# Kernel optimization log

Hardware: AMD Instinct MI355X
Metric: run time of the kernel (lower is better)

The kernel has to match this reference:

```python
import jax, jax.numpy as jnp
import numpy as np

B, S, D_IN, D_MODEL, H = 4, 2048, 1024, 1024, 16
D_HEAD = D_MODEL // H


def setup_inputs() -> dict:
    key = jax.random.key(0)
    ks = jax.random.split(key, 10)
    sc_in = 1.0 / np.sqrt(D_IN)
    sc_md = 1.0 / np.sqrt(D_MODEL)
    return {
        "X1": jax.random.normal(ks[0], (B, S, D_IN), jnp.float32),
        "X2": jax.random.normal(ks[1], (B, S, D_IN), jnp.float32),
        "Wq": jax.random.uniform(ks[2], (D_IN, D_MODEL), jnp.float32, -sc_in, sc_in),
        "bq": jax.random.uniform(ks[3], (D_MODEL,), jnp.float32, -sc_in, sc_in),
        "Wk": jax.random.uniform(ks[4], (D_IN, D_MODEL), jnp.float32, -sc_in, sc_in),
        "bk": jax.random.uniform(ks[5], (D_MODEL,), jnp.float32, -sc_in, sc_in),
        "Wv": jax.random.uniform(ks[6], (D_IN, D_MODEL), jnp.float32, -sc_in, sc_in),
        "bv": jax.random.uniform(ks[7], (D_MODEL,), jnp.float32, -sc_in, sc_in),
        "Wo": jax.random.uniform(ks[8], (D_MODEL, D_MODEL), jnp.float32, -sc_md, sc_md),
        "bo": jax.random.uniform(ks[9], (D_MODEL,), jnp.float32, -sc_md, sc_md),
    }


def _split_heads(x):
    b, s, _ = x.shape
    return x.reshape(b, s, H, D_HEAD).transpose(0, 2, 1, 3)  # [B,H,S,Dh]


def reference(X1, X2, Wq, bq, Wk, bk, Wv, bv, Wo, bo):
    Q = _split_heads(X1 @ Wq + bq)
    K = _split_heads(X2 @ Wk + bk)
    V = _split_heads(X2 @ Wv + bv)
    scale = 1.0 / np.sqrt(D_HEAD).astype(np.float32)
    # unfused attention: full [B,H,S,S] score matrix, as in the source
    scores = jnp.einsum("bhqd,bhkd->bhqk", Q, K) * scale
    attn = jax.nn.softmax(scores, axis=-1)
    out = jnp.einsum("bhqk,bhkd->bhqd", attn, V)
    out = out.transpose(0, 2, 1, 3).reshape(X1.shape[0], X1.shape[1], D_MODEL)
    return out @ Wo + bo
```

## Files before the change

### kernel.cpp

```cpp
#include <hip/hip_runtime.h>
#include <math.h>

typedef __bf16 bf16x8 __attribute__((ext_vector_type(8)));
typedef float  f32x4  __attribute__((ext_vector_type(4)));
typedef unsigned int uint2v __attribute__((ext_vector_type(2)));
typedef unsigned short u16;
typedef unsigned int   u32;

__device__ __forceinline__ u16 f2bf(float f) {
    u32 u = __builtin_bit_cast(u32, f);
    u32 r = (u + 0x7FFFu + ((u >> 16) & 1u)) >> 16;
    return (u16)r;
}

__device__ __forceinline__ u32 cvtpk_bf16(float lo, float hi) {
    u32 r;
    asm("v_cvt_pk_bf16_f32 %0, %1, %2" : "=v"(r) : "v"(lo), "v"(hi));
    return r;
}

#if __has_builtin(__builtin_amdgcn_exp2f)
__device__ __forceinline__ float fast_exp2(float x) { return __builtin_amdgcn_exp2f(x); }
#else
__device__ __forceinline__ float fast_exp2(float x) { return exp2f(x); }
#endif

__device__ __forceinline__ void mfma_16x16x16(f32x4& acc, uint2v a, uint2v b) {
    asm("v_mfma_f32_16x16x16_bf16 %0, %1, %2, %0" : "+v"(acc) : "v"(a), "v"(b));
}

__device__ __forceinline__ void gll16(const void* g, void* l) {
    __builtin_amdgcn_global_load_lds(
        (const __attribute__((address_space(1))) u32*)g,
        (__attribute__((address_space(3))) u32*)l, 16, 0, 0);
}

__device__ __forceinline__ f32x4 zero4() {
    f32x4 z; z[0] = 0.f; z[1] = 0.f; z[2] = 0.f; z[3] = 0.f; return z;
}

__global__ void cvt2_kernel(const float* __restrict__ in0, const float* __restrict__ in1,
                            u16* __restrict__ o0, u16* __restrict__ o1, int n) {
    const float* in = blockIdx.y ? in1 : in0;
    u16* out = blockIdx.y ? o1 : o0;
    int stride = gridDim.x * blockDim.x * 4;
    for (int i = (blockIdx.x * blockDim.x + threadIdx.x) * 4; i < n; i += stride) {
        float4 v = *(const float4*)&in[i];
        ushort4 r;
        r.x = f2bf(v.x); r.y = f2bf(v.y); r.z = f2bf(v.z); r.w = f2bf(v.w);
        *(ushort4*)&out[i] = r;
    }
}

__global__ void transpose_w(const float* __restrict__ W0, const float* __restrict__ W1,
                            const float* __restrict__ W2, const float* __restrict__ W3,
                            u16* __restrict__ T0, u16* __restrict__ T1,
                            u16* __restrict__ T2, u16* __restrict__ T3) {
    const float* W = blockIdx.z == 0 ? W0 : blockIdx.z == 1 ? W1 : blockIdx.z == 2 ? W2 : W3;
    u16*         T = blockIdx.z == 0 ? T0 : blockIdx.z == 1 ? T1 : blockIdx.z == 2 ? T2 : T3;
    __shared__ float tile[32][33];
    const int tx = threadIdx.x, ty = threadIdx.y;
    const int n0 = blockIdx.x * 32, k0 = blockIdx.y * 32;
#pragma unroll
    for (int i = 0; i < 4; ++i)
        tile[ty + 8 * i][tx] = W[(size_t)(k0 + ty + 8 * i) * 1024 + n0 + tx];
    __syncthreads();
#pragma unroll
    for (int i = 0; i < 4; ++i)
        T[(size_t)(n0 + ty + 8 * i) * 1024 + k0 + tx] = f2bf(tile[tx][ty + 8 * i]);
}

__global__ __launch_bounds__(256, 2)
void gemm_qkv(const u16* __restrict__ A1, const u16* __restrict__ A2,
              const u16* __restrict__ BTq, const u16* __restrict__ BTk, const u16* __restrict__ BTv,
              const float* __restrict__ bq, const float* __restrict__ bk, const float* __restrict__ bv,
              u16* __restrict__ qb, u16* __restrict__ kb, u16* __restrict__ vtb) {
    __shared__ u16 Alds[128 * 64];
    __shared__ u16 Blds[128 * 64];

    const int z = blockIdx.z;
    const u16* A    = z == 0 ? A1 : A2;
    const u16* BT   = z == 0 ? BTq : z == 1 ? BTk : BTv;
    const float* bias = z == 0 ? bq : z == 1 ? bk : bv;

    const int t = threadIdx.x;
    const int lane = t & 63, wid = t >> 6;
    const int wr = wid >> 1, wc = wid & 1;

    int wg = blockIdx.y * gridDim.x + blockIdx.x;
    const int cpx = 512 >> 3;
    wg = (wg & 7) * cpx + (wg >> 3);
    const int bx = wg & 7, by = wg >> 3;

    const int m0 = by * 128, n0 = bx * 128;

    f32x4 acc[4][4];
#pragma unroll
    for (int i = 0; i < 4; ++i)
#pragma unroll
        for (int j = 0; j < 4; ++j) acc[i][j] = zero4();

    const int srow = t >> 3;
    const int scol = (t & 7) * 8;
    const int lr = lane & 15;
    const int lk = (lane >> 4) * 8;

    for (int ko = 0; ko < 1024; ko += 64) {
#pragma unroll
        for (int i = 0; i < 4; ++i) {
            gll16(A  + (size_t)(m0 + srow + 32 * i) * 1024 + ko + scol, &Alds[(srow + 32 * i) * 64 + scol]);
            gll16(BT + (size_t)(n0 + srow + 32 * i) * 1024 + ko + scol, &Blds[(srow + 32 * i) * 64 + scol]);
        }
        __syncthreads();
#pragma unroll
        for (int kk = 0; kk < 2; ++kk) {
            bf16x8 a[4], b[4];
#pragma unroll
            for (int mi = 0; mi < 4; ++mi)
                a[mi] = *(const bf16x8*)&Alds[(wr * 64 + mi * 16 + lr) * 64 + kk * 32 + lk];
#pragma unroll
            for (int ni = 0; ni < 4; ++ni)
                b[ni] = *(const bf16x8*)&Blds[(wc * 64 + ni * 16 + lr) * 64 + kk * 32 + lk];
#pragma unroll
            for (int mi = 0; mi < 4; ++mi)
#pragma unroll
                for (int ni = 0; ni < 4; ++ni)
                    acc[mi][ni] = __builtin_amdgcn_mfma_f32_16x16x32_bf16(a[mi], b[ni], acc[mi][ni], 0, 0, 0);
        }
        __syncthreads();
    }

    const float KSC = (z == 1) ? 0.125f * 1.44269504f : 1.0f;

#pragma unroll
    for (int mi = 0; mi < 4; ++mi) {
#pragma unroll
        for (int ni = 0; ni < 4; ++ni) {
#pragma unroll
            for (int r = 0; r < 4; ++r) {
                const int m = m0 + wr * 64 + mi * 16 + (lane >> 4) * 4 + r;
                const int n = n0 + wc * 64 + ni * 16 + lr;
                const float v = (acc[mi][ni][r] + bias[n]) * KSC;
                const int b = m >> 11, s = m & 2047;
                const int hh = n >> 6, d = n & 63;
                const int bh = (b << 4) | hh;
                if (z <= 1) {
                    u16* dst = z == 0 ? qb : kb;
                    dst[((size_t)bh * 2048 + s) * 64 + d] = f2bf(v);
                } else {
                    vtb[((size_t)bh * 64 + d) * 2048 + s] = f2bf(v);
                }
            }
        }
    }
}

__global__ __launch_bounds__(256, 2)
void gemm_out(const u16* __restrict__ A, const u16* __restrict__ BT,
              const float* __restrict__ bias, float* __restrict__ out) {
    __shared__ u16 Alds[128 * 64];
    __shared__ u16 Blds[128 * 64];

    const int t = threadIdx.x;
    const int lane = t & 63, wid = t >> 6;
    const int wr = wid >> 1, wc = wid & 1;

    int wg = blockIdx.y * gridDim.x + blockIdx.x;
    const int cpx = 512 >> 3;
    wg = (wg & 7) * cpx + (wg >> 3);
    const int bx = wg & 7, by = wg >> 3;

    const int m0 = by * 128, n0 = bx * 128;

    f32x4 acc[4][4];
#pragma unroll
    for (int i = 0; i < 4; ++i)
#pragma unroll
        for (int j = 0; j < 4; ++j) acc[i][j] = zero4();

    const int srow = t >> 3;
    const int scol = (t & 7) * 8;
    const int lr = lane & 15;
    const int lk = (lane >> 4) * 8;

    for (int ko = 0; ko < 1024; ko += 64) {
#pragma unroll
        for (int i = 0; i < 4; ++i) {
            gll16(A  + (size_t)(m0 + srow + 32 * i) * 1024 + ko + scol, &Alds[(srow + 32 * i) * 64 + scol]);
            gll16(BT + (size_t)(n0 + srow + 32 * i) * 1024 + ko + scol, &Blds[(srow + 32 * i) * 64 + scol]);
        }
        __syncthreads();
#pragma unroll
        for (int kk = 0; kk < 2; ++kk) {
            bf16x8 a[4], b[4];
#pragma unroll
            for (int mi = 0; mi < 4; ++mi)
                a[mi] = *(const bf16x8*)&Alds[(wr * 64 + mi * 16 + lr) * 64 + kk * 32 + lk];
#pragma unroll
            for (int ni = 0; ni < 4; ++ni)
                b[ni] = *(const bf16x8*)&Blds[(wc * 64 + ni * 16 + lr) * 64 + kk * 32 + lk];
#pragma unroll
            for (int mi = 0; mi < 4; ++mi)
#pragma unroll
                for (int ni = 0; ni < 4; ++ni)
                    acc[mi][ni] = __builtin_amdgcn_mfma_f32_16x16x32_bf16(a[mi], b[ni], acc[mi][ni], 0, 0, 0);
        }
        __syncthreads();
    }

#pragma unroll
    for (int mi = 0; mi < 4; ++mi)
#pragma unroll
        for (int ni = 0; ni < 4; ++ni)
#pragma unroll
            for (int r = 0; r < 4; ++r) {
                const int m = m0 + wr * 64 + mi * 16 + (lane >> 4) * 4 + r;
                const int n = n0 + wc * 64 + ni * 16 + lr;
                out[(size_t)m * 1024 + n] = acc[mi][ni][r] + bias[n];
            }
}

__global__ __launch_bounds__(512, 4)
void attn_kernel(const u16* __restrict__ Q, const u16* __restrict__ K,
                 const u16* __restrict__ VT, u16* __restrict__ O) {
    __shared__ u16 Klds[64 * 64];
    __shared__ u16 Vlds[64 * 64];

    const int t = threadIdx.x;
    const int lane = t & 63, wid = t >> 6;
    const int bh = blockIdx.y;
    const int b = bh >> 4, h = bh & 15;
    const int q0 = blockIdx.x * 256 + wid * 32;

    const int lr = lane & 15;
    const int g  = lane >> 4;
    const int rdswz = (lr & 7) << 4;

    const u16* qb = Q + (size_t)bh * 2048 * 64;
    const u16* kb = K + (size_t)bh * 2048 * 64;
    const u16* vb = VT + (size_t)bh * 64 * 2048;

    bf16x8 qf[2][2];
#pragma unroll
    for (int nj = 0; nj < 2; ++nj)
#pragma unroll
        for (int kk = 0; kk < 2; ++kk)
            qf[nj][kk] = *(const bf16x8*)&qb[(size_t)(q0 + nj * 16 + lr) * 64 + kk * 32 + g * 8];

    f32x4 acco[2][4];
    float lsum[2];
#pragma unroll
    for (int nj = 0; nj < 2; ++nj) {
#pragma unroll
        for (int di = 0; di < 4; ++di) acco[nj][di] = zero4();
        lsum[nj] = 0.f;
    }

    const int srow = t >> 3;
    const int sb   = (t & 7) * 16;
    const int ssb  = sb ^ ((srow & 7) << 4);
    const int scolL = sb >> 1, scolG = ssb >> 1;

    for (int kt = 0; kt < 2048; kt += 64) {
        gll16(kb + (size_t)(kt + srow) * 64 + scolG, &Klds[srow * 64 + scolL]);
        gll16(vb + (size_t)srow * 2048 + kt + scolG, &Vlds[srow * 64 + scolL]);
        __syncthreads();

        f32x4 sc[2][4];
#pragma unroll
        for (int nj = 0; nj < 2; ++nj)
#pragma unroll
            for (int mi = 0; mi < 4; ++mi) sc[nj][mi] = zero4();
#pragma unroll
        for (int kk = 0; kk < 2; ++kk) {
            bf16x8 kf[4];
#pragma unroll
            for (int mi = 0; mi < 4; ++mi) {
                const int row = mi * 16 + lr;
                const int cb = (kk * 64 + g * 16) ^ rdswz;
                kf[mi] = *(const bf16x8*)&Klds[row * 64 + (cb >> 1)];
            }
#pragma unroll
            for (int nj = 0; nj < 2; ++nj)
#pragma unroll
                for (int mi = 0; mi < 4; ++mi)
                    sc[nj][mi] = __builtin_amdgcn_mfma_f32_16x16x32_bf16(kf[mi], qf[nj][kk], sc[nj][mi], 0, 0, 0);
        }

        uint2v pf[2][4];
#pragma unroll
        for (int nj = 0; nj < 2; ++nj) {
            float rs = 0.f;
#pragma unroll
            for (int mi = 0; mi < 4; ++mi) {
                const float p0 = fast_exp2(sc[nj][mi][0]);
                const float p1 = fast_exp2(sc[nj][mi][1]);
                const float p2 = fast_exp2(sc[nj][mi][2]);
                const float p3 = fast_exp2(sc[nj][mi][3]);
                rs += (p0 + p1) + (p2 + p3);
                pf[nj][mi][0] = cvtpk_bf16(p0, p1);
                pf[nj][mi][1] = cvtpk_bf16(p2, p3);
            }
            lsum[nj] += rs;
        }

#pragma unroll
        for (int di = 0; di < 4; ++di) {
#pragma unroll
            for (int mi = 0; mi < 4; ++mi) {
                const int row = di * 16 + lr;
                const int cb = (mi * 32 + g * 8) ^ rdswz;
                const uint2v vf = *(const uint2v*)&Vlds[row * 64 + (cb >> 1)];
#pragma unroll
                for (int nj = 0; nj < 2; ++nj)
                    mfma_16x16x16(acco[nj][di], vf, pf[nj][mi]);
            }
        }
        __syncthreads();
    }

#pragma unroll
    for (int nj = 0; nj < 2; ++nj) {
        float ls = lsum[nj];
        ls += __shfl_xor(ls, 16);
        ls += __shfl_xor(ls, 32);
        const float inv = 1.0f / ls;
        const size_t rowbase = ((size_t)b * 2048 + q0 + nj * 16 + lr) * 1024 + h * 64;
#pragma unroll
        for (int di = 0; di < 4; ++di) {
            uint2v w;
            w[0] = cvtpk_bf16(acco[nj][di][0] * inv, acco[nj][di][1] * inv);
            w[1] = cvtpk_bf16(acco[nj][di][2] * inv, acco[nj][di][3] * inv);
            *(uint2v*)&O[rowbase + di * 16 + g * 4] = w;
        }
    }
}

extern "C" void kernel_launch(void* const* d_in, const int* in_sizes, int n_in,
                              void* d_out, int out_size, void* d_ws, size_t ws_size,
                              hipStream_t stream) {
    const float* X1 = (const float*)d_in[0];
    const float* X2 = (const float*)d_in[1];
    const float* Wq = (const float*)d_in[2];
    const float* bq = (const float*)d_in[3];
    const float* Wk = (const float*)d_in[4];
    const float* bk = (const float*)d_in[5];
    const float* Wv = (const float*)d_in[6];
    const float* bv = (const float*)d_in[7];
    const float* Wo = (const float*)d_in[8];
    const float* bo = (const float*)d_in[9];
    float* out = (float*)d_out;

    char* ws = (char*)d_ws;
    const size_t MB = 1024 * 1024;
    u16* xb1 = (u16*)(ws);
    u16* xb2 = (u16*)(ws + 16 * MB);
    u16* wqT = (u16*)(ws + 32 * MB);
    u16* wkT = (u16*)(ws + 34 * MB);
    u16* wvT = (u16*)(ws + 36 * MB);
    u16* woT = (u16*)(ws + 38 * MB);
    u16* qb  = (u16*)(ws + 40 * MB);
    u16* kb  = (u16*)(ws + 56 * MB);
    u16* vtb = (u16*)(ws + 72 * MB);
    u16* ob  = (u16*)(ws + 88 * MB);

    cvt2_kernel<<<dim3(2048, 2), 256, 0, stream>>>(X1, X2, xb1, xb2, 8192 * 1024);
    transpose_w<<<dim3(32, 32, 4), dim3(32, 8), 0, stream>>>(Wq, Wk, Wv, Wo, wqT, wkT, wvT, woT);

    gemm_qkv<<<dim3(8, 64, 3), 256, 0, stream>>>(xb1, xb2, wqT, wkT, wvT, bq, bk, bv, qb, kb, vtb);

    attn_kernel<<<dim3(8, 64), 512, 0, stream>>>(qb, kb, vtb, ob);

    gemm_out<<<dim3(8, 64), 256, 0, stream>>>(ob, woT, bo, out);
}
```

Baseline: 210.6 us.

## Split attention key range across two blocks and add a combine kernel

The attention kernel now splits the 2048-key loop into two halves along a new grid z dimension. Each half writes an unnormalized bf16 numerator and its row sums into workspace that previously held the converted inputs and transposed weights, which are no longer needed at that point. A new elementwise combine kernel adds the two partials and divides by the summed denominators. The goal is to double the number of attention blocks so the GPU is better filled, at the cost of an extra kernel launch, extra memory traffic and one more bf16 rounding of the partial numerators.

New measurement: 223.8 us. 6.3% more time.

```diff
diff --git a/kernel.cpp b/kernel.cpp
--- a/kernel.cpp
+++ b/kernel.cpp
@@ -4,6 +4,7 @@
 typedef __bf16 bf16x8 __attribute__((ext_vector_type(8)));
 typedef float  f32x4  __attribute__((ext_vector_type(4)));
 typedef unsigned int uint2v __attribute__((ext_vector_type(2)));
+typedef unsigned int uint4v __attribute__((ext_vector_type(4)));
 typedef unsigned short u16;
 typedef unsigned int   u32;
 
@@ -222,15 +223,21 @@
 
 __global__ __launch_bounds__(512, 4)
 void attn_kernel(const u16* __restrict__ Q, const u16* __restrict__ K,
-                 const u16* __restrict__ VT, u16* __restrict__ O) {
+                 const u16* __restrict__ VT, u16* __restrict__ NUM,
+                 float* __restrict__ LSUM) {
     __shared__ u16 Klds[64 * 64];
     __shared__ u16 Vlds[64 * 64];
 
     const int t = threadIdx.x;
     const int lane = t & 63, wid = t >> 6;
     const int bh = blockIdx.y;
+    const int z = blockIdx.z;
     const int b = bh >> 4, h = bh & 15;
     const int q0 = blockIdx.x * 256 + wid * 32;
+    const int kbase = z * 1024;
+
+    u16* nb = NUM + (size_t)z * 4 * 2048 * 1024;
+    float* lb = LSUM + (size_t)z * 64 * 2048;
 
     const int lr = lane & 15;
     const int g  = lane >> 4;
@@ -261,7 +268,7 @@
     const int ssb  = sb ^ ((srow & 7) << 4);
     const int scolL = sb >> 1, scolG = ssb >> 1;
 
-    for (int kt = 0; kt < 2048; kt += 64) {
+    for (int kt = kbase; kt < kbase + 1024; kt += 64) {
         gll16(kb + (size_t)(kt + srow) * 64 + scolG, &Klds[srow * 64 + scolL]);
         gll16(vb + (size_t)srow * 2048 + kt + scolG, &Vlds[srow * 64 + scolL]);
         __syncthreads();
@@ -324,16 +331,47 @@
         float ls = lsum[nj];
         ls += __shfl_xor(ls, 16);
         ls += __shfl_xor(ls, 32);
-        const float inv = 1.0f / ls;
-        const size_t rowbase = ((size_t)b * 2048 + q0 + nj * 16 + lr) * 1024 + h * 64;
+        const int q = q0 + nj * 16 + lr;
+        if (g == 0) lb[(size_t)bh * 2048 + q] = ls;
+        const size_t rowbase = ((size_t)b * 2048 + q) * 1024 + h * 64;
 #pragma unroll
         for (int di = 0; di < 4; ++di) {
             uint2v w;
-            w[0] = cvtpk_bf16(acco[nj][di][0] * inv, acco[nj][di][1] * inv);
-            w[1] = cvtpk_bf16(acco[nj][di][2] * inv, acco[nj][di][3] * inv);
-            *(uint2v*)&O[rowbase + di * 16 + g * 4] = w;
-        }
-    }
+            w[0] = cvtpk_bf16(acco[nj][di][0], acco[nj][di][1]);
+            w[1] = cvtpk_bf16(acco[nj][di][2], acco[nj][di][3]);
+            *(uint2v*)&nb[rowbase + di * 16 + g * 4] = w;
+        }
+    }
+}
+
+__global__ __launch_bounds__(256)
+void combine_kernel(const u16* __restrict__ NUM, const float* __restrict__ LSUM,
+                    u16* __restrict__ O) {
+    const int i8 = blockIdx.x * 256 + threadIdx.x;
+    const int b = i8 >> 18;
+    const int rem = i8 & 262143;
+    const int s = rem >> 7;
+    const int dmc = rem & 127;
+    const int h = dmc >> 3;
+    const int bh = (b << 4) | h;
+
+    const size_t off = (size_t)i8 * 8;
+    const uint4v n0 = *(const uint4v*)&NUM[off];
+    const uint4v n1 = *(const uint4v*)&NUM[off + (size_t)4 * 2048 * 1024];
+    const float l = LSUM[(size_t)bh * 2048 + s] + LSUM[(size_t)(64 + bh) * 2048 + s];
+    const float inv = 1.0f / l;
+
+    uint4v w;
+#pragma unroll
+    for (int j = 0; j < 4; ++j) {
+        const u32 a = n0[j], c = n1[j];
+        const float lo = __builtin_bit_cast(float, (a & 0xFFFFu) << 16) +
+                         __builtin_bit_cast(float, (c & 0xFFFFu) << 16);
+        const float hi = __builtin_bit_cast(float, a & 0xFFFF0000u) +
+                         __builtin_bit_cast(float, c & 0xFFFF0000u);
+        w[j] = cvtpk_bf16(lo * inv, hi * inv);
+    }
+    *(uint4v*)&O[off] = w;
 }
 
 extern "C" void kernel_launch(void* const* d_in, const int* in_sizes, int n_in,
@@ -355,6 +393,8 @@
     const size_t MB = 1024 * 1024;
     u16* xb1 = (u16*)(ws);
     u16* xb2 = (u16*)(ws + 16 * MB);
+    u16* num = (u16*)(ws);
+    float* lsum = (float*)(ws + 32 * MB);
     u16* wqT = (u16*)(ws + 32 * MB);
     u16* wkT = (u16*)(ws + 34 * MB);
     u16* wvT = (u16*)(ws + 36 * MB);
@@ -369,7 +409,8 @@
 
     gemm_qkv<<<dim3(8, 64, 3), 256, 0, stream>>>(xb1, xb2, wqT, wkT, wvT, bq, bk, bv, qb, kb, vtb);
 
-    attn_kernel<<<dim3(8, 64), 512, 0, stream>>>(qb, kb, vtb, ob);
+    attn_kernel<<<dim3(8, 64, 2), 512, 0, stream>>>(qb, kb, vtb, num, lsum);
+    combine_kernel<<<4096, 256, 0, stream>>>(num, lsum, ob);
 
     gemm_out<<<dim3(8, 64), 256, 0, stream>>>(ob, woT, bo, out);
 }
```
